# Optimization experiments

Hardware: AMD Instinct MI355X
Metric: run time of the kernel (lower is better)

The kernel has to match this reference:

```python
import jax, jax.numpy as jnp
import numpy as np

DIM = 1024
HEADS = 16
DIM_HEAD = 64
DIM_INNER = HEADS * DIM_HEAD
SCALE = DIM_HEAD ** -0.5


def rmsnorm(x, w):
    eps = jnp.asarray(jnp.finfo(x.dtype).eps, x.dtype)
    var = jnp.mean(jnp.square(x), axis=-1, keepdims=True)
    return x * jax.lax.rsqrt(var + eps) * w


def setup_inputs() -> dict:
    key = jax.random.key(0)
    ks = jax.random.split(key, 6)
    tokens = jax.random.normal(ks[0], (2, 2048, DIM), dtype=jnp.float32)
    norm_w = jnp.ones((DIM,), dtype=jnp.float32)
    Wq = jax.random.normal(ks[1], (DIM, DIM_INNER), dtype=jnp.float32) * 0.02
    Wkv = jax.random.normal(ks[2], (DIM, 2 * DIM_INNER), dtype=jnp.float32) * 0.02
    Wout = jax.random.normal(ks[3], (DIM_INNER, DIM), dtype=jnp.float32) * 0.02
    Wg = jax.random.normal(ks[4], (DIM, HEADS), dtype=jnp.float32) * 0.02
    return {"tokens": tokens, "norm_w": norm_w, "Wq": Wq, "Wkv": Wkv, "Wout": Wout, "Wg": Wg}


def reference(tokens, norm_w, Wq, Wkv, Wout, Wg):
    b, n, _ = tokens.shape
    x = rmsnorm(tokens, norm_w)                      # [b, n, dim]
    q = x @ Wq                                       # [b, n, h*d]
    kv = x @ Wkv                                     # self-attention: context = tokens
    k, v = jnp.split(kv, 2, axis=-1)

    def split_heads(t):
        return t.reshape(b, n, HEADS, DIM_HEAD).transpose(0, 2, 1, 3)  # [b, h, n, d]

    q, k, v = map(split_heads, (q, k, v))

    sim = jnp.einsum('bhid,bhjd->bhij', q, k) * SCALE  # [b, h, n, n]
    causal_mask = jnp.triu(jnp.ones((n, n), dtype=bool), k=1)
    sim = jnp.where(causal_mask, jnp.asarray(-jnp.finfo(sim.dtype).max, sim.dtype), sim)
    attn = jax.nn.softmax(sim, axis=-1)
    out = jnp.einsum('bhij,bhjd->bhid', attn, v)       # [b, h, n, d]

    gates = jax.nn.sigmoid(x @ Wg)                     # [b, n, h]
    gates = gates.transpose(0, 2, 1)[..., None]        # [b, h, n, 1]
    out = gates * out

    out = out.transpose(0, 2, 1, 3).reshape(b, n, DIM_INNER)  # merge heads
    return out @ Wout                                  # [b, n, dim]
```

## Files before the change

### kernel.cpp

```cpp
#include <hip/hip_runtime.h>
#include <hip/hip_bf16.h>
#include <math.h>

constexpr int BB = 2;
constexpr int NN = 2048;
constexpr int DM = 1024;
constexpr int NH = 16;
constexpr int HD = 64;
constexpr int DI = NH * HD;
constexpr int MT = BB * NN;
constexpr float SM_SCALE = 0.125f * 1.44269504089f;

typedef __attribute__((ext_vector_type(8))) short short8v;
typedef __attribute__((ext_vector_type(4))) float f32x4;

__device__ inline unsigned cvt_pk_bf16(float lo, float hi) {
  unsigned r;
  asm("v_cvt_pk_bf16_f32 %0, %1, %2" : "=v"(r) : "v"(lo), "v"(hi));
  return r;
}
__device__ inline void pl32_swap(unsigned& a, unsigned& b) {
  asm("v_permlane32_swap_b32 %0, %1" : "+v"(a), "+v"(b));
}
__device__ inline void pl16_swap(unsigned& a, unsigned& b) {
  asm("v_permlane16_swap_b32 %0, %1" : "+v"(a), "+v"(b));
}
__device__ __forceinline__ void gload16(const void* g, void* l) {
  __builtin_amdgcn_global_load_lds(
      (const __attribute__((address_space(1))) unsigned int*)g,
      (__attribute__((address_space(3))) unsigned int*)l, 16, 0, 0);
}

__global__ __launch_bounds__(256) void k_prep(const float* __restrict__ tokens,
                                              const float* __restrict__ norm_w,
                                              const float* __restrict__ Wg,
                                              const float* __restrict__ Wq,
                                              const float* __restrict__ Wkv,
                                              const float* __restrict__ Wout,
                                              __hip_bfloat16* __restrict__ xb,
                                              float* __restrict__ g,
                                              __hip_bfloat16* __restrict__ Wqkvt,
                                              __hip_bfloat16* __restrict__ Woutt) {
  const int bid = blockIdx.x;
  const int t = threadIdx.x;
  if (bid < MT) {
    __shared__ float xs[DM];
    __shared__ float red[4];
    __shared__ float gred[4][16];
    const int tok = bid;
    float4 v = ((const float4*)(tokens + (size_t)tok * DM))[t];
    float ss = v.x * v.x + v.y * v.y + v.z * v.z + v.w * v.w;
#pragma unroll
    for (int m = 1; m < 64; m <<= 1) ss += __shfl_xor(ss, m, 64);
    if ((t & 63) == 0) red[t >> 6] = ss;
    __syncthreads();
    float tot = red[0] + red[1] + red[2] + red[3];
    float inv = rsqrtf(tot * (1.0f / DM) + 1.1920929e-7f);
    float4 wv = ((const float4*)norm_w)[t];
    float4 o;
    o.x = v.x * inv * wv.x;
    o.y = v.y * inv * wv.y;
    o.z = v.z * inv * wv.z;
    o.w = v.w * inv * wv.w;
    uint2 pk = make_uint2(cvt_pk_bf16(o.x, o.y), cvt_pk_bf16(o.z, o.w));
    *(uint2*)(xb + (size_t)tok * DM + t * 4) = pk;
    *(float4*)&xs[t * 4] = o;
    __syncthreads();
    const int h = t & 15, seg = t >> 4, wid = t >> 6;
    const float* xp = &xs[seg * 64];
    const float* wp = Wg + (size_t)(seg * 64) * NH + h;
    float s = 0.f;
#pragma unroll 8
    for (int k = 0; k < 64; k++) s = fmaf(xp[k], wp[(size_t)k * NH], s);
    s += __shfl_xor(s, 16);
    s += __shfl_xor(s, 32);
    if ((t & 63) < 16) gred[wid][h] = s;
    __syncthreads();
    if (t < 16) {
      float tot2 = gred[0][t] + gred[1][t] + gred[2][t] + gred[3][t];
      g[(size_t)tok * NH + t] = 1.f / (1.f + __expf(-tot2));
    }
  } else {
    const int wb = bid - MT;
    const int bx = wb & 127, by = wb >> 7;
    const int kb = by * 32;
    const float* W;
    __hip_bfloat16* dst;
    int N, col0, drow0;
    if (bx < 32) {
      W = Wq; N = DI; col0 = bx * 32; dst = Wqkvt; drow0 = col0;
    } else if (bx < 96) {
      W = Wkv; N = 2 * DI; col0 = (bx - 32) * 32; dst = Wqkvt; drow0 = DI + col0;
    } else {
      W = Wout; N = DM; col0 = (bx - 96) * 32; dst = Woutt; drow0 = col0;
    }
    __shared__ float tile[32][33];
    const int c = t & 31, r8 = t >> 5;
#pragma unroll
    for (int i = 0; i < 4; i++)
      tile[r8 + i * 8][c] = W[(size_t)(kb + r8 + i * 8) * N + col0 + c];
    __syncthreads();
#pragma unroll
    for (int i = 0; i < 4; i++)
      dst[(size_t)(drow0 + r8 + i * 8) * DM + kb + c] = __float2bfloat16(tile[c][r8 + i * 8]);
  }
}

template <int MODE>
__global__ __launch_bounds__(256) void k_mgemm(const __hip_bfloat16* __restrict__ A,
                                               const __hip_bfloat16* __restrict__ Bt,
                                               float* __restrict__ C,
                                               __hip_bfloat16* __restrict__ OQ,
                                               __hip_bfloat16* __restrict__ OK,
                                               __hip_bfloat16* __restrict__ OV, int Nc) {
  __shared__ __hip_bfloat16 As[128][32];
  __shared__ __hip_bfloat16 Bs[64][32];
  const int t = threadIdx.x, wid = t >> 6, lane = t & 63;
  const int lq = lane & 15, lg = lane >> 4;
  const int wr = wid >> 1, wc = wid & 1;
  const int m0 = blockIdx.y * 128, n0 = blockIdx.x * 64;
  const int srow = lane >> 2, scol = (lane & 3) * 8;

  const __hip_bfloat16* Ag = A + (size_t)(m0 + wid * 32 + srow) * DM + scol;
  const __hip_bfloat16* Bg = Bt + (size_t)(n0 + wid * 16 + srow) * DM + scol;

  f32x4 acc[4][2];
#pragma unroll
  for (int i = 0; i < 4; i++)
#pragma unroll
    for (int j = 0; j < 2; j++) acc[i][j] = (f32x4){0.f, 0.f, 0.f, 0.f};

  for (int k0 = 0; k0 < DM; k0 += 32) {
    __syncthreads();
    gload16(Ag + k0, &As[wid * 32][0]);
    gload16(Ag + 16 * DM + k0, &As[wid * 32 + 16][0]);
    gload16(Bg + k0, &Bs[wid * 16][0]);
    __syncthreads();
    short8v af[4], bf[2];
#pragma unroll
    for (int i = 0; i < 4; i++) af[i] = *(const short8v*)&As[wr * 64 + i * 16 + lq][lg * 8];
#pragma unroll
    for (int j = 0; j < 2; j++) bf[j] = *(const short8v*)&Bs[wc * 32 + j * 16 + lq][lg * 8];
#pragma unroll
    for (int i = 0; i < 4; i++)
#pragma unroll
      for (int j = 0; j < 2; j++)
        acc[i][j] = __builtin_amdgcn_mfma_f32_16x16x32_bf16(af[i], bf[j], acc[i][j], 0, 0, 0);
  }

#pragma unroll
  for (int i = 0; i < 4; i++) {
    const int mb = m0 + wr * 64 + i * 16 + lg * 4;
#pragma unroll
    for (int j = 0; j < 2; j++) {
      const int c = n0 + wc * 32 + j * 16 + lq;
      if (MODE == 0) {
#pragma unroll
        for (int r = 0; r < 4; r++) C[(size_t)(mb + r) * Nc + c] = acc[i][j][r];
      } else {
        const int b = mb >> 11, nl = mb & (NN - 1);
        if (c < DI) {
          const int h = c >> 6, d = c & 63;
          __hip_bfloat16* dst = OQ + ((size_t)(b * NH + h) * NN + nl) * HD + d;
#pragma unroll
          for (int r = 0; r < 4; r++) dst[(size_t)r * HD] = __float2bfloat16(acc[i][j][r]);
        } else if (c < 2 * DI) {
          const int ck = c - DI;
          const int h = ck >> 6, d = ck & 63;
          __hip_bfloat16* dst = OK + ((size_t)(b * NH + h) * NN + nl) * HD + d;
#pragma unroll
          for (int r = 0; r < 4; r++) dst[(size_t)r * HD] = __float2bfloat16(acc[i][j][r]);
        } else {
          const int cd = c - 2 * DI;
          const int h = cd >> 6, d = cd & 63;
          uint2 pk = make_uint2(cvt_pk_bf16(acc[i][j][0], acc[i][j][1]),
                                cvt_pk_bf16(acc[i][j][2], acc[i][j][3]));
          *(uint2*)(OV + ((size_t)(b * NH + h) * HD + d) * NN + nl) = pk;
        }
      }
    }
  }
}

__global__ __launch_bounds__(64) void k_attn_mfma(const __hip_bfloat16* __restrict__ Qb,
                                                  const __hip_bfloat16* __restrict__ Kb,
                                                  const __hip_bfloat16* __restrict__ Vtb,
                                                  const float* __restrict__ gates,
                                                  __hip_bfloat16* __restrict__ aob,
                                                  float* __restrict__ Opart,
                                                  float* __restrict__ mpart,
                                                  float* __restrict__ lpart) {
  const int bid = blockIdx.x;
  const int xcd = bid & 7;
  const int s = bid >> 3;
  const int gq = s / 96;
  const int t = s % 96;
  const int bh = gq * 8 + xcd;
  const int i = t / 3, j = t % 3;
  int grp, kt0, kt1, chunk;
  if (j < 2) {
    grp = 63 - i;
    chunk = j;
    const int nt = (grp >> 1) + 1;
    const int h0 = (nt + 1) >> 1;
    kt0 = chunk ? h0 : 0;
    kt1 = chunk ? nt : h0;
  } else {
    grp = 31 - i;
    chunk = -1;
    kt0 = 0;
    kt1 = (grp >> 1) + 1;
  }
  const int lane = threadIdx.x;
  const int lg = lane >> 4, lq = lane & 15;
  const int q0 = grp * 32;

  const __hip_bfloat16* Qh = Qb + (size_t)bh * NN * HD;
  const __hip_bfloat16* Kh = Kb + (size_t)bh * NN * HD;
  const __hip_bfloat16* Vh = Vtb + (size_t)bh * HD * NN;

  short8v qf0[2], qf1[2];
#pragma unroll
  for (int ks = 0; ks < 2; ks++) {
    qf0[ks] = *(const short8v*)(Qh + (size_t)(q0 + lq) * HD + ks * 32 + lg * 8);
    qf1[ks] = *(const short8v*)(Qh + (size_t)(q0 + 16 + lq) * HD + ks * 32 + lg * 8);
  }

  f32x4 oacc0[4], oacc1[4];
#pragma unroll
  for (int jx = 0; jx < 4; jx++) {
    oacc0[jx] = (f32x4){0.f, 0.f, 0.f, 0.f};
    oacc1[jx] = (f32x4){0.f, 0.f, 0.f, 0.f};
  }
  float m0r = -3.0e38f, l0p = 0.f, m1r = -3.0e38f, l1p = 0.f;

  auto LOADK = [&](short8v (*kf)[2], int kt) {
    const int kvb = kt * 64;
#pragma unroll
    for (int jx = 0; jx < 4; jx++)
#pragma unroll
      for (int ks = 0; ks < 2; ks++)
        kf[jx][ks] = *(const short8v*)(Kh + (size_t)(kvb + jx * 16 + lq) * HD + ks * 32 + lg * 8);
  };
  auto LOADV = [&](short8v (*vf)[2], int kt) {
    const int kvb = kt * 64;
#pragma unroll
    for (int jx = 0; jx < 4; jx++)
#pragma unroll
      for (int ks = 0; ks < 2; ks++)
        vf[jx][ks] = *(const short8v*)(Vh + (size_t)(jx * 16 + lq) * NN + kvb + ks * 32 + lg * 8);
  };

  auto GROUP = [&](const short8v* qf, f32x4* oacc, float& m_run, float& l_part,
                   int q0g, const short8v (*kf)[2], const short8v (*vf)[2], int kt) {
    const int kvb = kt * 64;
    f32x4 sacc[4];
#pragma unroll
    for (int jx = 0; jx < 4; jx++) sacc[jx] = (f32x4){0.f, 0.f, 0.f, 0.f};
#pragma unroll
    for (int jx = 0; jx < 4; jx++)
#pragma unroll
      for (int ks = 0; ks < 2; ks++)
        sacc[jx] = __builtin_amdgcn_mfma_f32_16x16x32_bf16(kf[jx][ks], qf[ks], sacc[jx], 0, 0, 0);

    const int qg = q0g + lq;
    const bool diag = (kvb + 63 > q0g);
    float ss[4][4];
#pragma unroll
    for (int jx = 0; jx < 4; jx++)
#pragma unroll
      for (int r = 0; r < 4; r++) {
        float v = sacc[jx][r] * SM_SCALE;
        if (diag && (kvb + jx * 16 + lg * 4 + r > qg)) v = -3.0e38f;
        ss[jx][r] = v;
      }

    float tmax = -3.0e38f;
#pragma unroll
    for (int jx = 0; jx < 4; jx++)
#pragma unroll
      for (int r = 0; r < 4; r++) tmax = fmaxf(tmax, ss[jx][r]);

    if (!__all(tmax <= m_run + 8.0f)) {
      float tr = fmaxf(tmax, __shfl_xor(tmax, 16));
      tr = fmaxf(tr, __shfl_xor(tr, 32));
      const float mnew = fmaxf(m_run, tr);
      const float cf = exp2f(m_run - mnew);
      l_part *= cf;
#pragma unroll
      for (int jx = 0; jx < 4; jx++)
#pragma unroll
        for (int r = 0; r < 4; r++) oacc[jx][r] *= cf;
      m_run = mnew;
    }

    float psum = 0.f;
    unsigned upk[4], vpk[4];
#pragma unroll
    for (int jx = 0; jx < 4; jx++) {
      float p0 = exp2f(ss[jx][0] - m_run), p1 = exp2f(ss[jx][1] - m_run);
      float p2 = exp2f(ss[jx][2] - m_run), p3 = exp2f(ss[jx][3] - m_run);
      psum += (p0 + p1) + (p2 + p3);
      upk[jx] = cvt_pk_bf16(p0, p1);
      vpk[jx] = cvt_pk_bf16(p2, p3);
    }
    l_part += psum;

#pragma unroll
    for (int ks = 0; ks < 2; ks++) {
      unsigned w0 = upk[2 * ks], w2 = upk[2 * ks + 1];
      unsigned w1 = vpk[2 * ks], w3 = vpk[2 * ks + 1];
      pl32_swap(w0, w2);
      pl16_swap(w0, w2);
      pl32_swap(w1, w3);
      pl16_swap(w1, w3);
      int4 bw = make_int4((int)w0, (int)w1, (int)w2, (int)w3);
      short8v pb = __builtin_bit_cast(short8v, bw);
#pragma unroll
      for (int jx = 0; jx < 4; jx++)
        oacc[jx] = __builtin_amdgcn_mfma_f32_16x16x32_bf16(vf[jx][ks], pb, oacc[jx], 0, 0, 0);
    }
  };

  short8v kfA[4][2], kfB[4][2], vf[4][2];
  LOADK(kfA, kt0);
  int kt = kt0;
  while (true) {
    LOADV(vf, kt);
    if (kt + 1 < kt1) LOADK(kfB, kt + 1);
    GROUP(qf0, oacc0, m0r, l0p, q0, kfA, vf, kt);
    GROUP(qf1, oacc1, m1r, l1p, q0 + 16, kfA, vf, kt);
    if (++kt == kt1) break;
    LOADV(vf, kt);
    if (kt + 1 < kt1) LOADK(kfA, kt + 1);
    GROUP(qf0, oacc0, m0r, l0p, q0, kfB, vf, kt);
    GROUP(qf1, oacc1, m1r, l1p, q0 + 16, kfB, vf, kt);
    if (++kt == kt1) break;
  }

  float l0 = l0p + __shfl_xor(l0p, 16);
  l0 += __shfl_xor(l0, 32);
  float l1 = l1p + __shfl_xor(l1p, 16);
  l1 += __shfl_xor(l1, 32);

  if (chunk >= 0) {
    const int gi = grp - 32;
    const size_t pidx = (size_t)(bh * 32 + gi) * 2 + chunk;
    float* Op = Opart + pidx * 2048;
#pragma unroll
    for (int jx = 0; jx < 4; jx++) {
      *(f32x4*)(Op + lq * 64 + jx * 16 + lg * 4) = oacc0[jx];
      *(f32x4*)(Op + (16 + lq) * 64 + jx * 16 + lg * 4) = oacc1[jx];
    }
    if (lane < 16) {
      mpart[pidx * 32 + lane] = m0r;
      mpart[pidx * 32 + 16 + lane] = m1r;
      lpart[pidx * 32 + lane] = l0;
      lpart[pidx * 32 + 16 + lane] = l1;
    }
    return;
  }

  const int b = bh >> 4, h = bh & 15;
  const float g0 = gates[((size_t)(b * NN + q0 + lq)) * NH + h];
  const float g1 = gates[((size_t)(b * NN + q0 + 16 + lq)) * NH + h];
  const float sc0 = g0 / l0, sc1 = g1 / l1;
  __shared__ float ots[32][68];
#pragma unroll
  for (int jx = 0; jx < 4; jx++)
#pragma unroll
    for (int r = 0; r < 4; r++) {
      ots[lq][jx * 16 + lg * 4 + r] = oacc0[jx][r] * sc0;
      ots[16 + lq][jx * 16 + lg * 4 + r] = oacc1[jx][r] * sc1;
    }
  __syncthreads();
  const int d0 = (lane & 3) * 16;
#pragma unroll
  for (int rr = 0; rr < 2; rr++) {
    const int rl = rr * 16 + (lane >> 2);
    __hip_bfloat16* aor = aob + ((size_t)(b * NN + q0 + rl)) * DI + h * HD + d0;
#pragma unroll
    for (int u = 0; u < 4; u++) {
      uint2 pk = make_uint2(
          cvt_pk_bf16(ots[rl][d0 + 4 * u + 0], ots[rl][d0 + 4 * u + 1]),
          cvt_pk_bf16(ots[rl][d0 + 4 * u + 2], ots[rl][d0 + 4 * u + 3]));
      *(uint2*)(aor + 4 * u) = pk;
    }
  }
}

__global__ __launch_bounds__(256) void k_attn_combine(const float* __restrict__ Opart,
                                                      const float* __restrict__ mpart,
                                                      const float* __restrict__ lpart,
                                                      const float* __restrict__ gates,
                                                      __hip_bfloat16* __restrict__ aob) {
  const int hg = blockIdx.x;
  const int h = hg >> 5, gi = hg & 31;
  const int grp = 32 + gi;
  const int t = threadIdx.x;
  const int row = t >> 3, dq = (t & 7) * 8;
  const size_t p0 = (size_t)hg * 2, p1 = p0 + 1;
  const float m0 = mpart[p0 * 32 + row], m1 = mpart[p1 * 32 + row];
  const float l0 = lpart[p0 * 32 + row], l1 = lpart[p1 * 32 + row];
  const float M = fmaxf(m0, m1);
  const float a0 = exp2f(m0 - M), a1 = exp2f(m1 - M);
  const float L = a0 * l0 + a1 * l1;
  const int b = h >> 4, hh = h & 15;
  const int grow = grp * 32 + row;
  const float sc = gates[((size_t)(b * NN + grow)) * NH + hh] / L;
  const float* O0 = Opart + p0 * 2048 + row * 64 + dq;
  const float* O1 = Opart + p1 * 2048 + row * 64 + dq;
  unsigned pk[4];
#pragma unroll
  for (int u = 0; u < 4; u++) {
    float x0 = (a0 * O0[2 * u + 0] + a1 * O1[2 * u + 0]) * sc;
    float x1 = (a0 * O0[2 * u + 1] + a1 * O1[2 * u + 1]) * sc;
    pk[u] = cvt_pk_bf16(x0, x1);
  }
  __hip_bfloat16* dst = aob + ((size_t)(b * NN + grow)) * DI + hh * 64 + dq;
  *(uint4*)dst = make_uint4(pk[0], pk[1], pk[2], pk[3]);
}

extern "C" void kernel_launch(void* const* d_in, const int* in_sizes, int n_in,
                              void* d_out, int out_size, void* d_ws, size_t ws_size,
                              hipStream_t stream) {
  const float* tokens = (const float*)d_in[0];
  const float* norm_w = (const float*)d_in[1];
  const float* Wq     = (const float*)d_in[2];
  const float* Wkv    = (const float*)d_in[3];
  const float* Wout   = (const float*)d_in[4];
  const float* Wg     = (const float*)d_in[5];
  float* out = (float*)d_out;

  float* ws = (float*)d_ws;
  float* gb = ws;
  __hip_bfloat16* xb    = (__hip_bfloat16*)(gb + (size_t)MT * NH);
  __hip_bfloat16* aob   = xb + (size_t)MT * DM;
  __hip_bfloat16* Qb    = aob + (size_t)MT * DM;
  __hip_bfloat16* Kb    = Qb + (size_t)MT * DI;
  __hip_bfloat16* Vtb   = Kb + (size_t)MT * DI;
  __hip_bfloat16* Wqkvt = Vtb + (size_t)MT * DI;
  __hip_bfloat16* Woutt = Wqkvt + (size_t)3 * DI * DM;
  float* Opart = (float*)(Woutt + (size_t)DM * DI);
  float* mpart = Opart + (size_t)2048 * 2048;
  float* lpart = mpart + (size_t)2048 * 32;

  k_prep<<<dim3(MT + 4096), 256, 0, stream>>>(tokens, norm_w, Wg, Wq, Wkv, Wout,
                                              xb, gb, Wqkvt, Woutt);
  k_mgemm<3><<<dim3(3 * DI / 64, MT / 128), 256, 0, stream>>>(
      xb, Wqkvt, nullptr, Qb, Kb, Vtb, 3 * DI);
  k_attn_mfma<<<dim3(32 * 96), 64, 0, stream>>>(Qb, Kb, Vtb, gb, aob, Opart, mpart, lpart);
  k_attn_combine<<<dim3(1024), 256, 0, stream>>>(Opart, mpart, lpart, gb, aob);
  k_mgemm<0><<<dim3(DM / 64, MT / 128), 256, 0, stream>>>(
      aob, Woutt, out, nullptr, nullptr, nullptr, DM);
}
```

Baseline: 167.8 us.

## Split attention KV range into 1-4 chunks per query group for better balance

Replaces the old two-way split of the upper half of query groups with graded split-KV: groups 48-63 get 4 chunks, 32-47 get 3, 16-31 get 2 and 0-15 stay whole. This spreads the causal triangle's work across more, more evenly sized blocks (5120 instead of 3072), aiming to cut tail imbalance. The combine kernel now merges a variable number of partials, and the workspace is re-laid out so the partial buffers alias xb/Wqkvt, which are dead by the time attention runs. The cost is more partial writes and reads and a larger combine launch.

```diff
diff --git a/kernel.cpp b/kernel.cpp
--- a/kernel.cpp
+++ b/kernel.cpp
@@ -193,24 +193,22 @@
   const int bid = blockIdx.x;
   const int xcd = bid & 7;
   const int s = bid >> 3;
-  const int gq = s / 96;
-  const int t = s % 96;
+  const int gq = s / 160;
+  const int tt = s % 160;
   const int bh = gq * 8 + xcd;
-  const int i = t / 3, j = t % 3;
-  int grp, kt0, kt1, chunk;
-  if (j < 2) {
-    grp = 63 - i;
-    chunk = j;
-    const int nt = (grp >> 1) + 1;
-    const int h0 = (nt + 1) >> 1;
-    kt0 = chunk ? h0 : 0;
-    kt1 = chunk ? nt : h0;
+  int grp, chunk, nc, base;
+  if (tt < 64) {
+    grp = 48 + (tt >> 2); chunk = tt & 3; nc = 4; base = 80 + (grp - 48) * 4;
+  } else if (tt < 112) {
+    const int u = tt - 64; grp = 32 + u / 3; chunk = u % 3; nc = 3; base = 32 + (grp - 32) * 3;
+  } else if (tt < 144) {
+    const int u = tt - 112; grp = 16 + (u >> 1); chunk = u & 1; nc = 2; base = (grp - 16) * 2;
   } else {
-    grp = 31 - i;
-    chunk = -1;
-    kt0 = 0;
-    kt1 = (grp >> 1) + 1;
-  }
+    grp = 15 - (tt - 144); chunk = -1; nc = 1; base = 0;
+  }
+  const int nt = (grp >> 1) + 1;
+  const int kt0 = (chunk >= 0) ? chunk * nt / nc : 0;
+  const int kt1 = (chunk >= 0) ? (chunk + 1) * nt / nc : nt;
   const int lane = threadIdx.x;
   const int lg = lane >> 4, lq = lane & 15;
   const int q0 = grp * 32;
@@ -344,8 +342,7 @@
   l1 += __shfl_xor(l1, 32);
 
   if (chunk >= 0) {
-    const int gi = grp - 32;
-    const size_t pidx = (size_t)(bh * 32 + gi) * 2 + chunk;
+    const size_t pidx = (size_t)bh * 144 + base + chunk;
     float* Op = Opart + pidx * 2048;
 #pragma unroll
     for (int jx = 0; jx < 4; jx++) {
@@ -395,28 +392,35 @@
                                                       const float* __restrict__ gates,
                                                       __hip_bfloat16* __restrict__ aob) {
   const int hg = blockIdx.x;
-  const int h = hg >> 5, gi = hg & 31;
-  const int grp = 32 + gi;
+  const int head = hg / 48, gi = hg % 48;
+  const int grp = 16 + gi;
+  int nc, base;
+  if (grp >= 48)      { nc = 4; base = 80 + (grp - 48) * 4; }
+  else if (grp >= 32) { nc = 3; base = 32 + (grp - 32) * 3; }
+  else                { nc = 2; base = (grp - 16) * 2; }
+  const size_t p0 = (size_t)head * 144 + base;
   const int t = threadIdx.x;
   const int row = t >> 3, dq = (t & 7) * 8;
-  const size_t p0 = (size_t)hg * 2, p1 = p0 + 1;
-  const float m0 = mpart[p0 * 32 + row], m1 = mpart[p1 * 32 + row];
-  const float l0 = lpart[p0 * 32 + row], l1 = lpart[p1 * 32 + row];
-  const float M = fmaxf(m0, m1);
-  const float a0 = exp2f(m0 - M), a1 = exp2f(m1 - M);
-  const float L = a0 * l0 + a1 * l1;
-  const int b = h >> 4, hh = h & 15;
+  float M = mpart[p0 * 32 + row];
+  for (int c = 1; c < nc; c++) M = fmaxf(M, mpart[(p0 + c) * 32 + row]);
+  float L = 0.f;
+  float acc[8] = {};
+  for (int c = 0; c < nc; c++) {
+    const float mc = mpart[(p0 + c) * 32 + row];
+    const float lc = lpart[(p0 + c) * 32 + row];
+    const float a = exp2f(mc - M);
+    L += a * lc;
+    const float* O = Opart + (p0 + c) * 2048 + row * 64 + dq;
+#pragma unroll
+    for (int u = 0; u < 8; u++) acc[u] = fmaf(a, O[u], acc[u]);
+  }
+  const int b = head >> 4, hh = head & 15;
   const int grow = grp * 32 + row;
   const float sc = gates[((size_t)(b * NN + grow)) * NH + hh] / L;
-  const float* O0 = Opart + p0 * 2048 + row * 64 + dq;
-  const float* O1 = Opart + p1 * 2048 + row * 64 + dq;
   unsigned pk[4];
 #pragma unroll
-  for (int u = 0; u < 4; u++) {
-    float x0 = (a0 * O0[2 * u + 0] + a1 * O1[2 * u + 0]) * sc;
-    float x1 = (a0 * O0[2 * u + 1] + a1 * O1[2 * u + 1]) * sc;
-    pk[u] = cvt_pk_bf16(x0, x1);
-  }
+  for (int u = 0; u < 4; u++)
+    pk[u] = cvt_pk_bf16(acc[2 * u] * sc, acc[2 * u + 1] * sc);
   __hip_bfloat16* dst = aob + ((size_t)(b * NN + grow)) * DI + hh * 64 + dq;
   *(uint4*)dst = make_uint4(pk[0], pk[1], pk[2], pk[3]);
 }
@@ -434,23 +438,23 @@
 
   float* ws = (float*)d_ws;
   float* gb = ws;
-  __hip_bfloat16* xb    = (__hip_bfloat16*)(gb + (size_t)MT * NH);
-  __hip_bfloat16* aob   = xb + (size_t)MT * DM;
+  __hip_bfloat16* aob   = (__hip_bfloat16*)(gb + (size_t)MT * NH);
   __hip_bfloat16* Qb    = aob + (size_t)MT * DM;
   __hip_bfloat16* Kb    = Qb + (size_t)MT * DI;
   __hip_bfloat16* Vtb   = Kb + (size_t)MT * DI;
-  __hip_bfloat16* Wqkvt = Vtb + (size_t)MT * DI;
-  __hip_bfloat16* Woutt = Wqkvt + (size_t)3 * DI * DM;
-  float* Opart = (float*)(Woutt + (size_t)DM * DI);
-  float* mpart = Opart + (size_t)2048 * 2048;
-  float* lpart = mpart + (size_t)2048 * 32;
+  __hip_bfloat16* Woutt = Vtb + (size_t)MT * DI;
+  float* mpart = (float*)(Woutt + (size_t)DM * DI);
+  float* lpart = mpart + (size_t)32 * 144 * 32;
+  float* Opart = lpart + (size_t)32 * 144 * 32;
+  __hip_bfloat16* xb    = (__hip_bfloat16*)Opart;
+  __hip_bfloat16* Wqkvt = xb + (size_t)MT * DM;
 
   k_prep<<<dim3(MT + 4096), 256, 0, stream>>>(tokens, norm_w, Wg, Wq, Wkv, Wout,
                                               xb, gb, Wqkvt, Woutt);
   k_mgemm<3><<<dim3(3 * DI / 64, MT / 128), 256, 0, stream>>>(
       xb, Wqkvt, nullptr, Qb, Kb, Vtb, 3 * DI);
-  k_attn_mfma<<<dim3(32 * 96), 64, 0, stream>>>(Qb, Kb, Vtb, gb, aob, Opart, mpart, lpart);
-  k_attn_combine<<<dim3(1024), 256, 0, stream>>>(Opart, mpart, lpart, gb, aob);
+  k_attn_mfma<<<dim3(32 * 160), 64, 0, stream>>>(Qb, Kb, Vtb, gb, aob, Opart, mpart, lpart);
+  k_attn_combine<<<dim3(32 * 48), 256, 0, stream>>>(Opart, mpart, lpart, gb, aob);
   k_mgemm<0><<<dim3(DM / 64, MT / 128), 256, 0, stream>>>(
       aob, Woutt, out, nullptr, nullptr, nullptr, DM);
 }
```

New measurement: 173.7 us. 3.5% more time.
